# Kernel tuning notes

Hardware: AMD Instinct MI355X
Metric: run time of the kernel (lower is better)

## Reference

```python
import jax, jax.numpy as jnp
import numpy as np

B, N, D = 2, 2048, 1024
H, DH = 16, 64
INNER = H * DH  # 1024
EPS = 1e-5


def setup_inputs() -> dict:
    key = jax.random.key(0)
    ks = jax.random.split(key, 7)
    x = jax.random.normal(ks[0], (B, N, D), dtype=jnp.float32)
    mask = jax.random.uniform(ks[1], (B, N)) < 0.9
    mask = mask.at[:, 0].set(True)  # guarantee at least one valid key per row
    attn_bias = jax.random.normal(ks[2], (H, N, N), dtype=jnp.float32) * 0.02
    ln_w = jnp.ones((D,), dtype=jnp.float32)
    ln_b = jnp.zeros((D,), dtype=jnp.float32)
    wq = jax.random.normal(ks[3], (D, INNER), dtype=jnp.float32) * 0.02
    wkv = jax.random.normal(ks[4], (D, 2 * DH), dtype=jnp.float32) * 0.02
    wo = jax.random.normal(ks[5], (INNER, D), dtype=jnp.float32) * 0.02
    return {"x": x, "attn_bias": attn_bias, "ln_w": ln_w, "ln_b": ln_b,
            "wq": wq, "wkv": wkv, "wo": wo, "mask": mask}


def reference(x, attn_bias, ln_w, ln_b, wq, wkv, wo, mask):
    scale = DH ** -0.5
    # NOTE: in the torch module, kv_input = x BEFORE self.norm (context=None),
    # so K/V come from raw x while Q comes from LayerNorm(x).
    mu = jnp.mean(x, axis=-1, keepdims=True)
    var = jnp.var(x, axis=-1, keepdims=True)
    xn = (x - mu) / jnp.sqrt(var + EPS) * ln_w + ln_b
    q = (xn @ wq).reshape(B, N, H, DH).transpose(0, 2, 1, 3) * scale  # b h n d
    kv = x @ wkv                     # b n 2*dh (shared single KV head, MQA)
    k, v = kv[..., :DH], kv[..., DH:]
    sim = jnp.einsum('bhid,bjd->bhij', q, k) + attn_bias  # bias broadcasts over b
    mask_value = -jnp.finfo(sim.dtype).max
    sim = jnp.where(mask[:, None, None, :], sim, mask_value)
    attn = jax.nn.softmax(sim, axis=-1)
    out = jnp.einsum('bhij,bjd->bhid', attn, v)
    out = out.transpose(0, 2, 1, 3).reshape(B, N, INNER)
    return out @ wo
```

## Files before the change

### kernel.cpp

```cpp
#include <hip/hip_runtime.h>
#include <hip/hip_bf16.h>

typedef __bf16 bf16_t;
typedef __bf16 bf16x4 __attribute__((ext_vector_type(4)));
typedef __bf16 bf16x8 __attribute__((ext_vector_type(8)));
typedef float f32x4 __attribute__((ext_vector_type(4)));

static constexpr int BB    = 2;
static constexpr int SEQ   = 2048;
static constexpr int DM    = 1024;
static constexpr int NHEAD = 16;
static constexpr int HD    = 64;
static constexpr float L2E = 1.4426950408889634f;

__device__ __forceinline__ bf16x8 ld8(const bf16_t* p) {
  return *reinterpret_cast<const bf16x8*>(p);
}

__device__ __forceinline__ void gl_lds16(const bf16_t* g, bf16_t* l) {
  __builtin_amdgcn_global_load_lds(
      (const __attribute__((address_space(1))) void*)g,
      (__attribute__((address_space(3))) void*)l, 16, 0, 0);
}

__device__ __forceinline__ uint2 shfl2(uint2 v, int src) {
  uint2 r;
  r.x = (unsigned)__shfl((int)v.x, src, 64);
  r.y = (unsigned)__shfl((int)v.y, src, 64);
  return r;
}

template <typename T> __device__ __forceinline__ T cvt_out(float v);
template <> __device__ __forceinline__ float  cvt_out<float >(float v) { return v; }
template <> __device__ __forceinline__ bf16_t cvt_out<bf16_t>(float v) { return (bf16_t)v; }

__device__ __forceinline__ void tc_body(const float* __restrict__ in,
                                        bf16_t* __restrict__ out,
                                        int R, int C, int bx, int by,
                                        float (*tile)[33]) {
  const int c0 = bx * 32, r0 = by * 32;
  const int tx = threadIdx.x & 31, ty = threadIdx.x >> 5;
#pragma unroll
  for (int y = ty; y < 32; y += 8)
    tile[y][tx] = in[(size_t)(r0 + y) * C + (c0 + tx)];
  __syncthreads();
#pragma unroll
  for (int y = ty; y < 32; y += 8)
    out[(size_t)(c0 + y) * R + (r0 + tx)] = (bf16_t)tile[tx][y];
}

__device__ __forceinline__ void row_prep_body(int row,
    const float* __restrict__ x, const float* __restrict__ ln_w,
    const float* __restrict__ ln_b, const int* __restrict__ mask,
    bf16_t* __restrict__ xbf, bf16_t* __restrict__ xn, float* __restrict__ maskA,
    float* red) {
  const int t = threadIdx.x;
  const float4 xv = *reinterpret_cast<const float4*>(&x[(size_t)row * DM + t * 4]);
  float s  = xv.x + xv.y + xv.z + xv.w;
  float s2 = xv.x * xv.x + xv.y * xv.y + xv.z * xv.z + xv.w * xv.w;
#pragma unroll
  for (int off = 32; off >= 1; off >>= 1) {
    s  += __shfl_xor(s,  off, 64);
    s2 += __shfl_xor(s2, off, 64);
  }
  if ((t & 63) == 0) { red[t >> 6] = s; red[4 + (t >> 6)] = s2; }
  __syncthreads();
  s  = red[0] + red[1] + red[2] + red[3];
  s2 = red[4] + red[5] + red[6] + red[7];
  const float mu   = s * (1.0f / DM);
  const float var  = s2 * (1.0f / DM) - mu * mu;
  const float rstd = rsqrtf(var + 1e-5f);
  const float4 wv = *reinterpret_cast<const float4*>(&ln_w[t * 4]);
  const float4 bv = *reinterpret_cast<const float4*>(&ln_b[t * 4]);
  union { bf16_t h[4]; uint2 u; } p0, p1;
  p0.h[0] = (bf16_t)xv.x; p0.h[1] = (bf16_t)xv.y;
  p0.h[2] = (bf16_t)xv.z; p0.h[3] = (bf16_t)xv.w;
  p1.h[0] = (bf16_t)((xv.x - mu) * rstd * wv.x + bv.x);
  p1.h[1] = (bf16_t)((xv.y - mu) * rstd * wv.y + bv.y);
  p1.h[2] = (bf16_t)((xv.z - mu) * rstd * wv.z + bv.z);
  p1.h[3] = (bf16_t)((xv.w - mu) * rstd * wv.w + bv.w);
  *reinterpret_cast<uint2*>(&xbf[(size_t)row * DM + t * 4]) = p0.u;
  *reinterpret_cast<uint2*>(&xn [(size_t)row * DM + t * 4]) = p1.u;
  if (t == 0) maskA[row] = mask[row] ? 0.0f : -1e30f;
}

__global__ __launch_bounds__(256) void prep_all(
    const float* __restrict__ x, const float* __restrict__ ln_w,
    const float* __restrict__ ln_b, const int* __restrict__ mask,
    const float* __restrict__ wq, const float* __restrict__ wkv,
    const float* __restrict__ wo,
    bf16_t* __restrict__ xbf, bf16_t* __restrict__ xn, float* __restrict__ maskA,
    bf16_t* __restrict__ wqT, bf16_t* __restrict__ wkvT, bf16_t* __restrict__ woT) {
  __shared__ float tile[32][33];
  __shared__ float red[8];
  const int bid = blockIdx.x;
  if (bid < 1024) {
    tc_body(wq, wqT, DM, DM, bid & 31, bid >> 5, tile);
  } else if (bid < 1152) {
    const int id = bid - 1024;
    tc_body(wkv, wkvT, DM, 128, id & 3, id >> 2, tile);
  } else if (bid < 2176) {
    const int id = bid - 1152;
    tc_body(wo, woT, DM, DM, id & 31, id >> 5, tile);
  } else {
    row_prep_body(bid - 2176, x, ln_w, ln_b, mask, xbf, xn, maskA, red);
  }
}

__device__ __forceinline__ void gemm_core_db(
    const bf16_t* __restrict__ A, const bf16_t* __restrict__ Bt, int K,
    int m0, int n0, bf16_t* As, bf16_t* Bs, f32x4 (&acc)[4][4]) {
  const int t = threadIdx.x, lane = t & 63, w = t >> 6;
  const int wm = (w & 1) * 64, wn = (w >> 1) * 64;
  const int l15 = lane & 15, q4 = lane >> 4;
  const int sr = lane >> 2, sc = (lane & 3) * 8;
  const bf16_t* Ap0 = A  + (size_t)(m0 + w * 32 + sr) * K + sc;
  const bf16_t* Ap1 = Ap0 + (size_t)16 * K;
  const bf16_t* Bp0 = Bt + (size_t)(n0 + w * 32 + sr) * K + sc;
  const bf16_t* Bp1 = Bp0 + (size_t)16 * K;
  const int la0 = (w * 32) * 32, la1 = (w * 32 + 16) * 32;
  gl_lds16(Ap0, As + la0);
  gl_lds16(Ap1, As + la1);
  gl_lds16(Bp0, Bs + la0);
  gl_lds16(Bp1, Bs + la1);
  __syncthreads();
  int buf = 0;
#pragma unroll 1
  for (int k0 = 0; k0 < K; k0 += 32) {
    const int nbuf = buf ^ 1;
    if (k0 + 32 < K) {
      const int kn = k0 + 32;
      gl_lds16(Ap0 + kn, As + nbuf * (128 * 32) + la0);
      gl_lds16(Ap1 + kn, As + nbuf * (128 * 32) + la1);
      gl_lds16(Bp0 + kn, Bs + nbuf * (128 * 32) + la0);
      gl_lds16(Bp1 + kn, Bs + nbuf * (128 * 32) + la1);
    }
    const bf16_t* Asb = As + buf * (128 * 32);
    const bf16_t* Bsb = Bs + buf * (128 * 32);
    bf16x8 af[4], bfr[4];
#pragma unroll
    for (int mt = 0; mt < 4; ++mt) af[mt]  = ld8(&Asb[(wm + mt * 16 + l15) * 32 + q4 * 8]);
#pragma unroll
    for (int nt = 0; nt < 4; ++nt) bfr[nt] = ld8(&Bsb[(wn + nt * 16 + l15) * 32 + q4 * 8]);
#pragma unroll
    for (int mt = 0; mt < 4; ++mt)
#pragma unroll
      for (int nt = 0; nt < 4; ++nt)
        acc[mt][nt] = __builtin_amdgcn_mfma_f32_16x16x32_bf16(af[mt], bfr[nt], acc[mt][nt], 0, 0, 0);
    __syncthreads();
    buf = nbuf;
  }
}

__global__ __launch_bounds__(256) void gemm_qkv(
    const bf16_t* __restrict__ xn,  const bf16_t* __restrict__ wqT,  bf16_t* __restrict__ qb,
    const bf16_t* __restrict__ xbf, const bf16_t* __restrict__ wkvT,
    bf16_t* __restrict__ kkb, bf16_t* __restrict__ vTb) {
  __shared__ alignas(16) bf16_t As[2][128 * 32];
  __shared__ alignas(16) bf16_t Bs[2][128 * 32];
  const int bx = blockIdx.x;
  const bool isKV = (bx < 32);
  const int m0 = isKV ? bx * 128 : ((bx - 32) & 31) * 128;
  const int n0 = isKV ? 0 : ((bx - 32) >> 5) * 128;
  const bf16_t* A  = isKV ? xbf  : xn;
  const bf16_t* Bt = isKV ? wkvT : wqT;
  f32x4 acc[4][4] = {};
  gemm_core_db(A, Bt, DM, m0, n0, &As[0][0], &Bs[0][0], acc);

  const int lane = threadIdx.x & 63, w = threadIdx.x >> 6;
  const int wm = (w & 1) * 64, wn = (w >> 1) * 64;
  const int l15 = lane & 15, q4 = lane >> 4;
#pragma unroll
  for (int mt = 0; mt < 4; ++mt)
#pragma unroll
    for (int nt = 0; nt < 4; ++nt)
#pragma unroll
      for (int r = 0; r < 4; ++r) {
        const int gm = m0 + wm + mt * 16 + q4 * 4 + r;
        const int gn = n0 + wn + nt * 16 + l15;
        if (isKV) {
          const bf16_t ov = (bf16_t)acc[mt][nt][r];
          if (gn < HD) kkb[(size_t)gm * HD + gn] = ov;
          else vTb[((size_t)(gm >> 11) * HD + (gn - HD)) * SEQ + (gm & 2047)] = ov;
        } else {
          qb[(size_t)gm * DM + gn] = (bf16_t)(acc[mt][nt][r] * 0.125f);
        }
      }
}

__global__ __launch_bounds__(256) void gemm_out(const bf16_t* __restrict__ A,
    const bf16_t* __restrict__ Bt, float* __restrict__ C, int K) {
  __shared__ alignas(16) bf16_t As[2][128 * 32];
  __shared__ alignas(16) bf16_t Bs[2][128 * 32];
  const int m0 = blockIdx.x * 128, n0 = blockIdx.y * 128;
  f32x4 acc[4][4] = {};
  gemm_core_db(A, Bt, K, m0, n0, &As[0][0], &Bs[0][0], acc);
  const int lane = threadIdx.x & 63, w = threadIdx.x >> 6;
  const int wm = (w & 1) * 64, wn = (w >> 1) * 64;
  const int l15 = lane & 15, q4 = lane >> 4;
#pragma unroll
  for (int mt = 0; mt < 4; ++mt)
#pragma unroll
    for (int nt = 0; nt < 4; ++nt)
#pragma unroll
      for (int r = 0; r < 4; ++r) {
        const int gm = m0 + wm + mt * 16 + q4 * 4 + r;
        const int gn = n0 + wn + nt * 16 + l15;
        C[(size_t)gm * DM + gn] = acc[mt][nt][r];
      }
}

__global__ __launch_bounds__(256, 4) void flash_attn(
    const bf16_t* __restrict__ q,
    const bf16_t* __restrict__ kk,
    const bf16_t* __restrict__ vT,
    const float*  __restrict__ bias,
    const float*  __restrict__ maskA,
    bf16_t* __restrict__ aout)
{
  const int b = blockIdx.y & 1, h = blockIdx.y >> 1;
  const int i0 = blockIdx.x * 64;
  const int t = threadIdx.x, lane = t & 63, w = t >> 6;
  const int l15 = lane & 15, q4 = lane >> 4;

  __shared__ alignas(16) bf16_t Ks[2][64][72];
  __shared__ alignas(16) bf16_t Vs[2][64][72];

  const bf16_t* qrow = &q[((size_t)b * SEQ + i0 + w * 16 + l15) * DM + h * HD];
  const bf16x8 bq0 = ld8(qrow + q4 * 8);
  const bf16x8 bq1 = ld8(qrow + 32 + q4 * 8);

  f32x4 o[4] = {};
  float m_run = -1e30f, l_run = 0.0f;

  const float* bias_p = bias + (size_t)h * SEQ * SEQ
                      + (size_t)(i0 + w * 16 + l15) * SEQ + q4 * 4;
  const float* mask_p = maskA + b * SEQ + q4 * 4;

  const int sr = t >> 2, sc = (t & 3) * 16;
  const bf16_t* kp = &kk[((size_t)b * SEQ + sr) * HD + sc];
  const bf16_t* vp = &vT[((size_t)b * HD + sr) * SEQ + sc];

  uint4 kr0 = *reinterpret_cast<const uint4*>(kp);
  uint4 kr1 = *reinterpret_cast<const uint4*>(kp + 8);
  uint4 vr0 = *reinterpret_cast<const uint4*>(vp);
  uint4 vr1 = *reinterpret_cast<const uint4*>(vp + 8);
  f32x4 bv[4], mv[4];
#pragma unroll
  for (int mt = 0; mt < 4; ++mt) {
    bv[mt] = *reinterpret_cast<const f32x4*>(bias_p + mt * 16);
    mv[mt] = *reinterpret_cast<const f32x4*>(mask_p + mt * 16);
  }
  *reinterpret_cast<uint4*>(&Ks[0][sr][sc])     = kr0;
  *reinterpret_cast<uint4*>(&Ks[0][sr][sc + 8]) = kr1;
  *reinterpret_cast<uint4*>(&Vs[0][sr][sc])     = vr0;
  *reinterpret_cast<uint4*>(&Vs[0][sr][sc + 8]) = vr1;
  __syncthreads();

  for (int it = 0; it < SEQ / 64; ++it) {
    const int buf = it & 1;
    const int j1 = (it + 1) * 64;
    const bool more = (j1 < SEQ);
    if (more) {
      kr0 = *reinterpret_cast<const uint4*>(kp + (size_t)j1 * HD);
      kr1 = *reinterpret_cast<const uint4*>(kp + (size_t)j1 * HD + 8);
      vr0 = *reinterpret_cast<const uint4*>(vp + j1);
      vr1 = *reinterpret_cast<const uint4*>(vp + j1 + 8);
    }

    f32x4 s[4];
#pragma unroll
    for (int mt = 0; mt < 4; ++mt) {
      const bf16x8 a0 = ld8(&Ks[buf][mt * 16 + l15][q4 * 8]);
      const bf16x8 a1 = ld8(&Ks[buf][mt * 16 + l15][32 + q4 * 8]);
      f32x4 z = {0.f, 0.f, 0.f, 0.f};
      z = __builtin_amdgcn_mfma_f32_16x16x32_bf16(a0, bq0, z, 0, 0, 0);
      z = __builtin_amdgcn_mfma_f32_16x16x32_bf16(a1, bq1, z, 0, 0, 0);
      s[mt] = z;
    }

    float mx = -1e30f;
#pragma unroll
    for (int mt = 0; mt < 4; ++mt)
#pragma unroll
      for (int r = 0; r < 4; ++r) {
        s[mt][r] = s[mt][r] + bv[mt][r] + mv[mt][r];
        mx = fmaxf(mx, s[mt][r]);
      }
    if (more) {
#pragma unroll
      for (int mt = 0; mt < 4; ++mt) {
        bv[mt] = *reinterpret_cast<const f32x4*>(bias_p + j1 + mt * 16);
        mv[mt] = *reinterpret_cast<const f32x4*>(mask_p + j1 + mt * 16);
      }
    }
    mx = fmaxf(mx, __shfl_xor(mx, 16, 64));
    mx = fmaxf(mx, __shfl_xor(mx, 32, 64));
    const float mnew  = fmaxf(m_run, mx);
    const float alpha = __builtin_amdgcn_exp2f((m_run - mnew) * L2E);
    const float cc    = -mnew * L2E;
    m_run = mnew;

    float su = 0.0f;
#pragma unroll
    for (int mt = 0; mt < 4; ++mt)
#pragma unroll
      for (int r = 0; r < 4; ++r) {
        s[mt][r] = __builtin_amdgcn_exp2f(__builtin_fmaf(s[mt][r], L2E, cc));
        su += s[mt][r];
      }
    su += __shfl_xor(su, 16, 64);
    su += __shfl_xor(su, 32, 64);
    l_run = l_run * alpha + su;

#pragma unroll
    for (int r = 0; r < 4; ++r) {
      const float a_r = __shfl(alpha, q4 * 4 + r, 64);
      o[0][r] *= a_r; o[1][r] *= a_r; o[2][r] *= a_r; o[3][r] *= a_r;
    }

    uint2 pk[4];
#pragma unroll
    for (int mt = 0; mt < 4; ++mt) {
      union { bf16_t hh[4]; uint2 u; } pu;
      pu.hh[0] = (bf16_t)s[mt][0]; pu.hh[1] = (bf16_t)s[mt][1];
      pu.hh[2] = (bf16_t)s[mt][2]; pu.hh[3] = (bf16_t)s[mt][3];
      pk[mt] = pu.u;
    }
    const int src0 = ((q4 & 1) << 5) + l15;
    const int src1 = src0 + 16;
    const bool hiSel = (q4 >> 1) != 0;
#pragma unroll
    for (int ks = 0; ks < 2; ++ks) {
      const uint2 a0 = shfl2(pk[2 * ks],     src0);
      const uint2 a1 = shfl2(pk[2 * ks + 1], src0);
      const uint2 b0 = shfl2(pk[2 * ks],     src1);
      const uint2 b1 = shfl2(pk[2 * ks + 1], src1);
      union { unsigned u[4]; bf16x8 v; } pf;
      pf.u[0] = hiSel ? a1.x : a0.x; pf.u[1] = hiSel ? a1.y : a0.y;
      pf.u[2] = hiSel ? b1.x : b0.x; pf.u[3] = hiSel ? b1.y : b0.y;
#pragma unroll
      for (int nt = 0; nt < 4; ++nt) {
        const bf16x8 vv = ld8(&Vs[buf][nt * 16 + l15][ks * 32 + q4 * 8]);
        o[nt] = __builtin_amdgcn_mfma_f32_16x16x32_bf16(pf.v, vv, o[nt], 0, 0, 0);
      }
    }

    if (more) {
      *reinterpret_cast<uint4*>(&Ks[buf ^ 1][sr][sc])     = kr0;
      *reinterpret_cast<uint4*>(&Ks[buf ^ 1][sr][sc + 8]) = kr1;
      *reinterpret_cast<uint4*>(&Vs[buf ^ 1][sr][sc])     = vr0;
      *reinterpret_cast<uint4*>(&Vs[buf ^ 1][sr][sc + 8]) = vr1;
    }
    __syncthreads();
  }

#pragma unroll
  for (int r = 0; r < 4; ++r) {
    const float linv = 1.0f / __shfl(l_run, q4 * 4 + r, 64);
    const int gi = i0 + w * 16 + q4 * 4 + r;
    bf16_t* dst = &aout[((size_t)b * SEQ + gi) * DM + h * HD];
#pragma unroll
    for (int nt = 0; nt < 4; ++nt)
      dst[nt * 16 + l15] = (bf16_t)(o[nt][r] * linv);
  }
}

extern "C" void kernel_launch(void* const* d_in, const int* in_sizes, int n_in,
                              void* d_out, int out_size, void* d_ws, size_t ws_size,
                              hipStream_t stream) {
  const float* x         = (const float*)d_in[0];
  const float* attn_bias = (const float*)d_in[1];
  const float* ln_w      = (const float*)d_in[2];
  const float* ln_b      = (const float*)d_in[3];
  const float* wq        = (const float*)d_in[4];
  const float* wkv       = (const float*)d_in[5];
  const float* wo        = (const float*)d_in[6];
  const int*   mask      = (const int*)d_in[7];
  float* out = (float*)d_out;

  char* ws = (char*)d_ws;
  size_t off = 0;
  auto alloc = [&](size_t bytes) {
    char* p = ws + off;
    off += (bytes + 255) & ~(size_t)255;
    return p;
  };
  bf16_t* xbf   = (bf16_t*)alloc((size_t)BB * SEQ * DM * 2);
  bf16_t* xn    = (bf16_t*)alloc((size_t)BB * SEQ * DM * 2);
  bf16_t* wqT   = (bf16_t*)alloc((size_t)DM * DM * 2);
  bf16_t* wkvT  = (bf16_t*)alloc((size_t)2 * HD * DM * 2);
  bf16_t* woT   = (bf16_t*)alloc((size_t)DM * DM * 2);
  bf16_t* qb    = (bf16_t*)alloc((size_t)BB * SEQ * DM * 2);
  bf16_t* kkb   = (bf16_t*)alloc((size_t)BB * SEQ * HD * 2);
  bf16_t* vTb   = (bf16_t*)alloc((size_t)BB * HD * SEQ * 2);
  bf16_t* aoutb = (bf16_t*)alloc((size_t)BB * SEQ * DM * 2);
  float*  maskA = (float*)alloc((size_t)BB * SEQ * 4);

  prep_all<<<6272, 256, 0, stream>>>(x, ln_w, ln_b, mask, wq, wkv, wo,
                                     xbf, xn, maskA, wqT, wkvT, woT);
  gemm_qkv<<<288, 256, 0, stream>>>(xn, wqT, qb, xbf, wkvT, kkb, vTb);
  flash_attn<<<dim3(SEQ / 64, BB * NHEAD), 256, 0, stream>>>(qb, kkb, vTb, attn_bias,
                                                             maskA, aoutb);
  gemm_out<<<dim3(32, 8), 256, 0, stream>>>(aoutb, woT, out, DM);
}
```

Baseline: 479.3 us.

## Switch flash attention to 32x32x16 MFMA with 128-row query tiles

```diff
diff --git a/kernel.cpp b/kernel.cpp
--- a/kernel.cpp
+++ b/kernel.cpp
@@ -5,6 +5,7 @@
 typedef __bf16 bf16x4 __attribute__((ext_vector_type(4)));
 typedef __bf16 bf16x8 __attribute__((ext_vector_type(8)));
 typedef float f32x4 __attribute__((ext_vector_type(4)));
+typedef float f32x16 __attribute__((ext_vector_type(16)));
 
 static constexpr int BB    = 2;
 static constexpr int SEQ   = 2048;
@@ -21,13 +22,6 @@
   __builtin_amdgcn_global_load_lds(
       (const __attribute__((address_space(1))) void*)g,
       (__attribute__((address_space(3))) void*)l, 16, 0, 0);
-}
-
-__device__ __forceinline__ uint2 shfl2(uint2 v, int src) {
-  uint2 r;
-  r.x = (unsigned)__shfl((int)v.x, src, 64);
-  r.y = (unsigned)__shfl((int)v.y, src, 64);
-  return r;
 }
 
 template <typename T> __device__ __forceinline__ T cvt_out(float v);
@@ -210,7 +204,7 @@
       }
 }
 
-__global__ __launch_bounds__(256, 4) void flash_attn(
+__global__ __launch_bounds__(256, 2) void flash_attn(
     const bf16_t* __restrict__ q,
     const bf16_t* __restrict__ kk,
     const bf16_t* __restrict__ vT,
@@ -219,23 +213,25 @@
     bf16_t* __restrict__ aout)
 {
   const int b = blockIdx.y & 1, h = blockIdx.y >> 1;
-  const int i0 = blockIdx.x * 64;
+  const int i0 = blockIdx.x * 128;
   const int t = threadIdx.x, lane = t & 63, w = t >> 6;
-  const int l15 = lane & 15, q4 = lane >> 4;
+  const int l31 = lane & 31, hi = lane >> 5;
 
   __shared__ alignas(16) bf16_t Ks[2][64][72];
   __shared__ alignas(16) bf16_t Vs[2][64][72];
 
-  const bf16_t* qrow = &q[((size_t)b * SEQ + i0 + w * 16 + l15) * DM + h * HD];
-  const bf16x8 bq0 = ld8(qrow + q4 * 8);
-  const bf16x8 bq1 = ld8(qrow + 32 + q4 * 8);
-
-  f32x4 o[4] = {};
+  const int qrow = i0 + w * 32 + l31;
+  const bf16_t* qp = &q[((size_t)b * SEQ + qrow) * DM + h * HD];
+  bf16x8 qf[4];
+#pragma unroll
+  for (int st = 0; st < 4; ++st) qf[st] = ld8(qp + st * 16 + hi * 8);
+
+  f32x16 o0 = {}, o1 = {};
   float m_run = -1e30f, l_run = 0.0f;
 
-  const float* bias_p = bias + (size_t)h * SEQ * SEQ
-                      + (size_t)(i0 + w * 16 + l15) * SEQ + q4 * 4;
-  const float* mask_p = maskA + b * SEQ + q4 * 4;
+  const float* bias_p = bias + (size_t)h * SEQ * SEQ + (size_t)qrow * SEQ;
+  const float* mask_p = maskA + b * SEQ;
+  const int boff = 4 * hi;
 
   const int sr = t >> 2, sc = (t & 3) * 16;
   const bf16_t* kp = &kk[((size_t)b * SEQ + sr) * HD + sc];
@@ -245,18 +241,22 @@
   uint4 kr1 = *reinterpret_cast<const uint4*>(kp + 8);
   uint4 vr0 = *reinterpret_cast<const uint4*>(vp);
   uint4 vr1 = *reinterpret_cast<const uint4*>(vp + 8);
-  f32x4 bv[4], mv[4];
-#pragma unroll
-  for (int mt = 0; mt < 4; ++mt) {
-    bv[mt] = *reinterpret_cast<const f32x4*>(bias_p + mt * 16);
-    mv[mt] = *reinterpret_cast<const f32x4*>(mask_p + mt * 16);
-  }
+  f32x4 bm[2][4];
+#pragma unroll
+  for (int kt = 0; kt < 2; ++kt)
+#pragma unroll
+    for (int g = 0; g < 4; ++g) {
+      const int ko = kt * 32 + g * 8 + boff;
+      bm[kt][g] = *reinterpret_cast<const f32x4*>(bias_p + ko)
+                + *reinterpret_cast<const f32x4*>(mask_p + ko);
+    }
   *reinterpret_cast<uint4*>(&Ks[0][sr][sc])     = kr0;
   *reinterpret_cast<uint4*>(&Ks[0][sr][sc + 8]) = kr1;
   *reinterpret_cast<uint4*>(&Vs[0][sr][sc])     = vr0;
   *reinterpret_cast<uint4*>(&Vs[0][sr][sc + 8]) = vr1;
   __syncthreads();
 
+#pragma unroll 1
   for (int it = 0; it < SEQ / 64; ++it) {
     const int buf = it & 1;
     const int j1 = (it + 1) * 64;
@@ -268,33 +268,32 @@
       vr1 = *reinterpret_cast<const uint4*>(vp + j1 + 8);
     }
 
-    f32x4 s[4];
-#pragma unroll
-    for (int mt = 0; mt < 4; ++mt) {
-      const bf16x8 a0 = ld8(&Ks[buf][mt * 16 + l15][q4 * 8]);
-      const bf16x8 a1 = ld8(&Ks[buf][mt * 16 + l15][32 + q4 * 8]);
-      f32x4 z = {0.f, 0.f, 0.f, 0.f};
-      z = __builtin_amdgcn_mfma_f32_16x16x32_bf16(a0, bq0, z, 0, 0, 0);
-      z = __builtin_amdgcn_mfma_f32_16x16x32_bf16(a1, bq1, z, 0, 0, 0);
-      s[mt] = z;
+    f32x16 s0 = {}, s1 = {};
+#pragma unroll
+    for (int st = 0; st < 4; ++st) {
+      const bf16x8 kf0 = ld8(&Ks[buf][l31]     [st * 16 + hi * 8]);
+      const bf16x8 kf1 = ld8(&Ks[buf][32 + l31][st * 16 + hi * 8]);
+      s0 = __builtin_amdgcn_mfma_f32_32x32x16_bf16(kf0, qf[st], s0, 0, 0, 0);
+      s1 = __builtin_amdgcn_mfma_f32_32x32x16_bf16(kf1, qf[st], s1, 0, 0, 0);
     }
 
     float mx = -1e30f;
 #pragma unroll
-    for (int mt = 0; mt < 4; ++mt)
-#pragma unroll
-      for (int r = 0; r < 4; ++r) {
-        s[mt][r] = s[mt][r] + bv[mt][r] + mv[mt][r];
-        mx = fmaxf(mx, s[mt][r]);
-      }
+    for (int r = 0; r < 16; ++r) {
+      s0[r] = s0[r] + bm[0][r >> 2][r & 3];
+      s1[r] = s1[r] + bm[1][r >> 2][r & 3];
+      mx = fmaxf(mx, fmaxf(s0[r], s1[r]));
+    }
     if (more) {
 #pragma unroll
-      for (int mt = 0; mt < 4; ++mt) {
-        bv[mt] = *reinterpret_cast<const f32x4*>(bias_p + j1 + mt * 16);
-        mv[mt] = *reinterpret_cast<const f32x4*>(mask_p + j1 + mt * 16);
-      }
-    }
-    mx = fmaxf(mx, __shfl_xor(mx, 16, 64));
+      for (int kt = 0; kt < 2; ++kt)
+#pragma unroll
+        for (int g = 0; g < 4; ++g) {
+          const int ko = j1 + kt * 32 + g * 8 + boff;
+          bm[kt][g] = *reinterpret_cast<const f32x4*>(bias_p + ko)
+                    + *reinterpret_cast<const f32x4*>(mask_p + ko);
+        }
+    }
     mx = fmaxf(mx, __shfl_xor(mx, 32, 64));
     const float mnew  = fmaxf(m_run, mx);
     const float alpha = __builtin_amdgcn_exp2f((m_run - mnew) * L2E);
@@ -303,47 +302,46 @@
 
     float su = 0.0f;
 #pragma unroll
-    for (int mt = 0; mt < 4; ++mt)
-#pragma unroll
-      for (int r = 0; r < 4; ++r) {
-        s[mt][r] = __builtin_amdgcn_exp2f(__builtin_fmaf(s[mt][r], L2E, cc));
-        su += s[mt][r];
-      }
-    su += __shfl_xor(su, 16, 64);
+    for (int r = 0; r < 16; ++r) {
+      s0[r] = __builtin_amdgcn_exp2f(__builtin_fmaf(s0[r], L2E, cc));
+      s1[r] = __builtin_amdgcn_exp2f(__builtin_fmaf(s1[r], L2E, cc));
+      su += s0[r] + s1[r];
+    }
     su += __shfl_xor(su, 32, 64);
     l_run = l_run * alpha + su;
 
 #pragma unroll
-    for (int r = 0; r < 4; ++r) {
-      const float a_r = __shfl(alpha, q4 * 4 + r, 64);
-      o[0][r] *= a_r; o[1][r] *= a_r; o[2][r] *= a_r; o[3][r] *= a_r;
-    }
-
-    uint2 pk[4];
-#pragma unroll
-    for (int mt = 0; mt < 4; ++mt) {
-      union { bf16_t hh[4]; uint2 u; } pu;
-      pu.hh[0] = (bf16_t)s[mt][0]; pu.hh[1] = (bf16_t)s[mt][1];
-      pu.hh[2] = (bf16_t)s[mt][2]; pu.hh[3] = (bf16_t)s[mt][3];
-      pk[mt] = pu.u;
-    }
-    const int src0 = ((q4 & 1) << 5) + l15;
-    const int src1 = src0 + 16;
-    const bool hiSel = (q4 >> 1) != 0;
-#pragma unroll
-    for (int ks = 0; ks < 2; ++ks) {
-      const uint2 a0 = shfl2(pk[2 * ks],     src0);
-      const uint2 a1 = shfl2(pk[2 * ks + 1], src0);
-      const uint2 b0 = shfl2(pk[2 * ks],     src1);
-      const uint2 b1 = shfl2(pk[2 * ks + 1], src1);
-      union { unsigned u[4]; bf16x8 v; } pf;
-      pf.u[0] = hiSel ? a1.x : a0.x; pf.u[1] = hiSel ? a1.y : a0.y;
-      pf.u[2] = hiSel ? b1.x : b0.x; pf.u[3] = hiSel ? b1.y : b0.y;
-#pragma unroll
-      for (int nt = 0; nt < 4; ++nt) {
-        const bf16x8 vv = ld8(&Vs[buf][nt * 16 + l15][ks * 32 + q4 * 8]);
-        o[nt] = __builtin_amdgcn_mfma_f32_16x16x32_bf16(pf.v, vv, o[nt], 0, 0, 0);
+    for (int r = 0; r < 16; ++r) { o0[r] *= alpha; o1[r] *= alpha; }
+
+    bf16x8 pf[4];
+#pragma unroll
+    for (int w16 = 0; w16 < 4; ++w16) {
+      const int st2 = w16 & 1;
+      const f32x16& sv = (w16 < 2) ? s0 : s1;
+      union { bf16_t hh[4]; unsigned u[2]; } A, Bu;
+#pragma unroll
+      for (int j = 0; j < 4; ++j) {
+        A.hh[j]  = (bf16_t)sv[st2 * 8 + j];
+        Bu.hh[j] = (bf16_t)sv[st2 * 8 + 4 + j];
       }
+      const unsigned x0 = hi ? A.u[0] : Bu.u[0];
+      const unsigned x1 = hi ? A.u[1] : Bu.u[1];
+      const unsigned y0 = (unsigned)__shfl_xor((int)x0, 32, 64);
+      const unsigned y1 = (unsigned)__shfl_xor((int)x1, 32, 64);
+      union { unsigned u[4]; bf16x8 v; } P;
+      P.u[0] = hi ? y0 : A.u[0];
+      P.u[1] = hi ? y1 : A.u[1];
+      P.u[2] = hi ? Bu.u[0] : y0;
+      P.u[3] = hi ? Bu.u[1] : y1;
+      pf[w16] = P.v;
+    }
+
+#pragma unroll
+    for (int w16 = 0; w16 < 4; ++w16) {
+      const bf16x8 vf0 = ld8(&Vs[buf][l31]     [w16 * 16 + hi * 8]);
+      const bf16x8 vf1 = ld8(&Vs[buf][32 + l31][w16 * 16 + hi * 8]);
+      o0 = __builtin_amdgcn_mfma_f32_32x32x16_bf16(vf0, pf[w16], o0, 0, 0, 0);
+      o1 = __builtin_amdgcn_mfma_f32_32x32x16_bf16(vf1, pf[w16], o1, 0, 0, 0);
     }
 
     if (more) {
@@ -355,14 +353,18 @@
     __syncthreads();
   }
 
-#pragma unroll
-  for (int r = 0; r < 4; ++r) {
-    const float linv = 1.0f / __shfl(l_run, q4 * 4 + r, 64);
-    const int gi = i0 + w * 16 + q4 * 4 + r;
-    bf16_t* dst = &aout[((size_t)b * SEQ + gi) * DM + h * HD];
-#pragma unroll
-    for (int nt = 0; nt < 4; ++nt)
-      dst[nt * 16 + l15] = (bf16_t)(o[nt][r] * linv);
+  const float linv = 1.0f / l_run;
+  bf16_t* dst = &aout[((size_t)b * SEQ + qrow) * DM + h * HD];
+#pragma unroll
+  for (int g = 0; g < 4; ++g) {
+    union { bf16_t hh[4]; uint2 u2; } E0, E1;
+#pragma unroll
+    for (int j = 0; j < 4; ++j) {
+      E0.hh[j] = (bf16_t)(o0[g * 4 + j] * linv);
+      E1.hh[j] = (bf16_t)(o1[g * 4 + j] * linv);
+    }
+    *reinterpret_cast<uint2*>(dst + g * 8 + 4 * hi)      = E0.u2;
+    *reinterpret_cast<uint2*>(dst + 32 + g * 8 + 4 * hi) = E1.u2;
   }
 }
 
@@ -400,7 +402,7 @@
   prep_all<<<6272, 256, 0, stream>>>(x, ln_w, ln_b, mask, wq, wkv, wo,
                                      xbf, xn, maskA, wqT, wkvT, woT);
   gemm_qkv<<<288, 256, 0, stream>>>(xn, wqT, qb, xbf, wkvT, kkb, vTb);
-  flash_attn<<<dim3(SEQ / 64, BB * NHEAD), 256, 0, stream>>>(qb, kkb, vTb, attn_bias,
-                                                             maskA, aoutb);
+  flash_attn<<<dim3(SEQ / 128, BB * NHEAD), 256, 0, stream>>>(qb, kkb, vTb, attn_bias,
+                                                              maskA, aoutb);
   gemm_out<<<dim3(32, 8), 256, 0, stream>>>(aoutb, woT, out, DM);
 }
```

New measurement: 491.7 us. +2.6%, slower.
